# Kernel optimization log

Measured on AMD Instinct MI355X. Metric: run time of the kernel, lower is better.

The kernel has to match this reference:

```python
import jax, jax.numpy as jnp
from jax import lax
import numpy as np

MSS = 1448.0
MAX_RTT = 0.01
B, S = 2048, 4096


def setup_inputs() -> dict:
    key = jax.random.key(0)
    k1, k2, k3, k4 = jax.random.split(key, 4)
    # packet lengths in [0, 1500) bytes so bursts aggregate past MSS=1448
    x = jax.random.uniform(k1, (B, S), jnp.float32) * 1500.0
    mask = jax.random.uniform(k2, (B, S)) < 0.1
    scale = 0.00094557476340694
    d_exp = 1e-6 + scale * jax.random.exponential(k3, (B, S), jnp.float32)
    delays = jnp.where(mask, jnp.float32(0.21), d_exp)
    # per-burst RTT samples, indexed by the burst-start packet position
    rtts = jax.random.uniform(k4, (B, S), jnp.float32) * MAX_RTT
    return {"x": x, "delays": delays, "rtts": rtts}


def _simulate_row(x, delays, rtts):
    # x, delays, rtts: [S]
    S_ = x.shape[0]

    def step(carry, inp):
        active, new_burst, r = carry
        xj, dj, rj = inp
        # outer-while check only at burst start: stop forever if x[j] <= 0
        active = jnp.where(new_burst, active & (xj > 0), active)
        r = jnp.where(new_burst, rj, r)
        r_next = r - dj  # inner while: RTT -= delays[j]
        burst_end = active & (r_next <= 0)
        start_flag = new_burst & active
        return (active, burst_end, r_next), (active, start_flag)

    init = (jnp.bool_(True), jnp.bool_(True), jnp.float32(0.0))
    _, (consumed, start_flag) = lax.scan(step, init, (x, delays, rtts))

    # per-burst buffered byte count: segment-sum of consumed packet lengths
    burst_id = jnp.clip(jnp.cumsum(start_flag.astype(jnp.int32)) - 1, 0, S_ - 1)
    buf = jax.ops.segment_sum(jnp.where(consumed, x, 0.0), burst_id, num_segments=S_)

    # `while buf > MSS` emits ceil(buf/MSS)-1 full segments, then remainder
    n_full = jnp.maximum(jnp.ceil(buf / MSS).astype(jnp.int32) - 1, 0)
    rem = buf - n_full.astype(x.dtype) * MSS
    has_rem = rem > 0
    count = n_full + has_rem.astype(jnp.int32)
    starts = jnp.cumsum(count) - count  # exclusive cumsum: output offset per burst
    ends = starts + n_full

    # difference-array trick: positions in [starts, ends) get MSS (OOB drops == truncation)
    diff = (jnp.zeros(S_, jnp.int32)
            .at[starts].add(1, mode='drop')
            .at[ends].add(-1, mode='drop'))
    cover = jnp.cumsum(diff) > 0
    out = jnp.where(cover, jnp.float32(MSS), jnp.float32(0.0))

    # remainder goes right after the MSS run of its burst
    rem_pos = jnp.where(has_rem, ends, S_)  # S_ -> dropped
    out = out.at[rem_pos].set(rem, mode='drop')
    return out


def reference(x, delays, rtts):
    out = jax.vmap(_simulate_row)(x, delays, rtts)  # [B, S]
    return out[..., None]  # unsqueeze(-1) -> [B, S, 1]
```

## Files before the change

### kernel.cpp

```cpp
#include <hip/hip_runtime.h>
#include <math.h>


#define S_LEN 4096
#define BLOCK 512
#define PER   8
#define MSSF  1448.0f

#define OFF_A    0
#define OFF_JB   8208
#define OFF_NXT  16416
#define OFF_MENT 24616
#define OFF_WS   25640
#define SMEM_SZ  25672

__device__ __forceinline__ int s2i(int p) { return p ^ (((p >> 6) & 15) << 1); }

__global__ __launch_bounds__(BLOCK, 8) void traffic_kernel(
    const float* __restrict__ gx,
    const float* __restrict__ gd,
    const float* __restrict__ gr,
    float* __restrict__ gout)
{
    __shared__ __align__(16) unsigned char smem[SMEM_SZ];
    float*          s_dly  = (float*)(smem + OFF_A);
    unsigned short* s_jA   = (unsigned short*)(smem + OFF_A);
    unsigned short* s_jB   = (unsigned short*)(smem + OFF_JB);
    int*            s_diff = (int*)(smem + OFF_A);
    float*          s_out  = (float*)(smem + OFF_A);
    unsigned short* s_nxt  = (unsigned short*)(smem + OFF_NXT);
    unsigned short* s_ment = (unsigned short*)(smem + OFF_MENT);
    int*            s_ws   = (int*)(smem + OFF_WS);

    const int tid = threadIdx.x;
    const size_t rowoff = (size_t)blockIdx.x * S_LEN;
    const float* px = gx + rowoff;
    const float* pd = gd + rowoff;
    const float* pr = gr + rowoff;

    {
        const float4* pd4 = (const float4*)pd;
        float4* s4 = (float4*)s_dly;
        for (int q = tid; q < S_LEN / 4; q += BLOCK) s4[q] = pd4[q];
        if (tid < 8) s_dly[S_LEN + tid] = 1.0e30f;
    }
    float rt[PER];
    unsigned alive = 0;
#pragma unroll
    for (int i = 0; i < PER; ++i) rt[i] = pr[tid + (i << 9)];
#pragma unroll
    for (int i = 0; i < PER; ++i) alive |= (px[tid + (i << 9)] > 0.0f) ? (1u << i) : 0u;
    __syncthreads();

    unsigned surv = 0;
    float rsv[PER];
#pragma unroll
    for (int i = 0; i < PER; ++i) {
        const int p0 = tid + (i << 9);
        const float* dw = s_dly + p0;
        float d0 = dw[0], d1 = dw[1], d2 = dw[2], d3 = dw[3];
        float d4 = dw[4], d5 = dw[5], d6 = dw[6], d7 = dw[7];
        float r1 = rt[i] - d0;
        float r2 = r1 - d1;
        float r3 = r2 - d2;
        float r4 = r3 - d3;
        float r5 = r4 - d4;
        float r6 = r5 - d5;
        float r7 = r6 - d6;
        float r8 = r7 - d7;
        int c = (r1 > 0.0f) + (r2 > 0.0f) + (r3 > 0.0f) + (r4 > 0.0f) +
                (r5 > 0.0f) + (r6 > 0.0f) + (r7 > 0.0f) + (r8 > 0.0f);
        rsv[i] = r8;
        bool al = (alive >> i) & 1u;
        if (al && c == 8) {
            surv |= 1u << i;
        } else {
            int nx = al ? (p0 + c + 1) : S_LEN;
            if (nx > S_LEN) nx = S_LEN;
            s_nxt[s2i(p0)] = (unsigned short)nx;
        }
    }

    while (surv) {
        int i = __ffs(surv) - 1;
        surv &= surv - 1;
        float rr = rsv[0];
#pragma unroll
        for (int ii = 1; ii < PER; ++ii) rr = (i == ii) ? rsv[ii] : rr;
        int p0 = tid + (i << 9);
        int j = p0 + 8;
        int nx;
        while (true) {
            float e0 = s_dly[j],     e1 = s_dly[j + 1];
            float e2 = s_dly[j + 2], e3 = s_dly[j + 3];
            float e4 = s_dly[j + 4], e5 = s_dly[j + 5];
            float e6 = s_dly[j + 6], e7 = s_dly[j + 7];
            float q1 = rr - e0;
            float q2 = q1 - e1;
            float q3 = q2 - e2;
            float q4 = q3 - e3;
            float q5 = q4 - e4;
            float q6 = q5 - e5;
            float q7 = q6 - e6;
            float q8 = q7 - e7;
            int c2 = (q1 > 0.0f) + (q2 > 0.0f) + (q3 > 0.0f) + (q4 > 0.0f) +
                     (q5 > 0.0f) + (q6 > 0.0f) + (q7 > 0.0f) + (q8 > 0.0f);
            if (c2 < 8) { nx = j + c2 + 1; break; }
            j += 8;
            rr = q8;
        }
        if (nx > S_LEN) nx = S_LEN;
        s_nxt[s2i(p0)] = (unsigned short)nx;
    }
    __syncthreads();

    const int sb = tid << 3;
    {
        int nv[PER], ee[PER];
#pragma unroll
        for (int i = 0; i < PER; ++i) nv[i] = (int)s_nxt[s2i(sb + i)];
#pragma unroll
        for (int i = PER - 1; i >= 0; --i) {
            int v = nv[i];
            int e = v;
#pragma unroll
            for (int j2 = i + 1; j2 < PER; ++j2)
                if (v == sb + j2) e = ee[j2];
            ee[i] = e;
        }
        uint4 pk;
        pk.x = (unsigned)ee[0] | ((unsigned)ee[1] << 16);
        pk.y = (unsigned)ee[2] | ((unsigned)ee[3] << 16);
        pk.z = (unsigned)ee[4] | ((unsigned)ee[5] << 16);
        pk.w = (unsigned)ee[6] | ((unsigned)ee[7] << 16);
        *(uint4*)&s_jA[sb] = pk;
    }
    if (tid == 0) { s_jA[4096] = (unsigned short)4096; s_jB[4096] = (unsigned short)4096; }
    s_ment[tid] = (tid == 0) ? (unsigned short)1 : (unsigned short)0;
    __syncthreads();

    {
        unsigned short* ja = s_jA;
        unsigned short* jb = s_jB;
        int own[PER];
#pragma unroll
        for (int i = 0; i < PER; ++i) own[i] = (int)ja[tid + (i << 9)];
        for (int k = 0; k < 9; ++k) {
            int ent = (int)s_ment[tid];
            int q = -1;
            if (ent) {
                int e = (int)ja[ent - 1];
                if (e < S_LEN) q = e;
            }
            if (k < 8) {
                int nv[PER];
#pragma unroll
                for (int i = 0; i < PER; ++i) nv[i] = (int)ja[own[i]];
                if (q >= 0) s_ment[q >> 3] = (unsigned short)(q + 1);
#pragma unroll
                for (int i = 0; i < PER; ++i) jb[tid + (i << 9)] = (unsigned short)nv[i];
#pragma unroll
                for (int i = 0; i < PER; ++i) own[i] = nv[i];
            } else {
                if (q >= 0) s_ment[q >> 3] = (unsigned short)(q + 1);
            }
            __syncthreads();
            unsigned short* t = ja; ja = jb; jb = t;
        }
    }

    unsigned lm = 0;
    {
        int ent = (int)s_ment[tid];
        if (ent) {
            int p = ent - 1;
            while (p < sb + PER) {
                lm |= 1u << (p - sb);
                p = (int)s_nxt[s2i(p)];
            }
        }
    }

    float bsum[PER];
    unsigned use = 0;
    int tsum = 0;
#pragma unroll
    for (int i = 0; i < PER; ++i) {
        float buf = 0.0f;
        int c = 0;
        if ((lm >> i) & 1u) {
            int p = sb + i;
            float xp = px[p];
            if (xp > 0.0f) {
                use |= 1u << i;
                int e = (int)s_nxt[s2i(p)];
                float sum = xp;
                for (int j = p + 1; j < e; ++j) sum += px[j];
                buf = sum;
                int nf = (int)ceilf(buf / MSSF) - 1; if (nf < 0) nf = 0;
                float rem = buf - (float)nf * MSSF;
                c = nf + (rem > 0.0f ? 1 : 0);
            }
        }
        bsum[i] = buf;
        tsum += c;
    }

    int texcl;
    {
        int lane = tid & 63, wv = tid >> 6;
        int v = tsum;
        for (int off = 1; off < 64; off <<= 1) {
            int u = __shfl_up(v, off, 64);
            if (lane >= off) v += u;
        }
        if (lane == 63) s_ws[wv] = v;
        __syncthreads();
        int woff = 0;
        for (int w = 0; w < wv; ++w) woff += s_ws[w];
        texcl = woff + v - tsum;
    }

    {
        int4* d4 = (int4*)s_diff;
        int4 z; z.x = z.y = z.z = z.w = 0;
        d4[tid] = z;
        d4[tid + 512] = z;
    }
    __syncthreads();

    {
        int o = texcl;
#pragma unroll
        for (int i = 0; i < PER; ++i) {
            if ((use >> i) & 1u) {
                float buf = bsum[i];
                int nf = (int)ceilf(buf / MSSF) - 1; if (nf < 0) nf = 0;
                float rem = buf - (float)nf * MSSF;
                if (nf > 0) {
                    if (o < S_LEN) atomicAdd(&s_diff[o], 1);
                    int e2 = o + nf;
                    if (e2 < S_LEN) atomicAdd(&s_diff[e2], -1);
                }
                o += nf + (rem > 0.0f ? 1 : 0);
            }
        }
    }
    __syncthreads();

    {
        int4 a = *(int4*)&s_diff[sb];
        int4 b = *(int4*)&s_diff[sb + 4];
        int v0 = a.x,      v1 = v0 + a.y, v2 = v1 + a.z, v3 = v2 + a.w;
        int v4 = v3 + b.x, v5 = v4 + b.y, v6 = v5 + b.z, v7 = v6 + b.w;
        int T = v7;
        int lane = tid & 63, wv = tid >> 6;
        int sc = T;
        for (int off = 1; off < 64; off <<= 1) {
            int u = __shfl_up(sc, off, 64);
            if (lane >= off) sc += u;
        }
        if (lane == 63) s_ws[wv] = sc;
        __syncthreads();
        int basev = 0;
        for (int w = 0; w < wv; ++w) basev += s_ws[w];
        basev += sc - T;
        float4 fa, fb;
        fa.x = (basev + v0 > 0) ? MSSF : 0.0f;
        fa.y = (basev + v1 > 0) ? MSSF : 0.0f;
        fa.z = (basev + v2 > 0) ? MSSF : 0.0f;
        fa.w = (basev + v3 > 0) ? MSSF : 0.0f;
        fb.x = (basev + v4 > 0) ? MSSF : 0.0f;
        fb.y = (basev + v5 > 0) ? MSSF : 0.0f;
        fb.z = (basev + v6 > 0) ? MSSF : 0.0f;
        fb.w = (basev + v7 > 0) ? MSSF : 0.0f;
        *(float4*)&s_out[sb]     = fa;
        *(float4*)&s_out[sb + 4] = fb;
    }
    __syncthreads();

    {
        int o = texcl;
#pragma unroll
        for (int i = 0; i < PER; ++i) {
            if ((use >> i) & 1u) {
                float buf = bsum[i];
                int nf = (int)ceilf(buf / MSSF) - 1; if (nf < 0) nf = 0;
                float rem = buf - (float)nf * MSSF;
                int rp = o + nf;
                if (rem > 0.0f && rp < S_LEN) s_out[rp] = rem;
                o += nf + (rem > 0.0f ? 1 : 0);
            }
        }
    }
    __syncthreads();

    {
        float4* po4 = (float4*)(gout + rowoff);
        const float4* so4 = (const float4*)s_out;
        po4[tid]       = so4[tid];
        po4[tid + 512] = so4[tid + 512];
    }
}

extern "C" void kernel_launch(void* const* d_in, const int* in_sizes, int n_in,
                              void* d_out, int out_size, void* d_ws, size_t ws_size,
                              hipStream_t stream) {
    const float* x      = (const float*)d_in[0];
    const float* delays = (const float*)d_in[1];
    const float* rtts   = (const float*)d_in[2];
    float* out = (float*)d_out;
    int rows = in_sizes[0] / S_LEN;
    traffic_kernel<<<rows, BLOCK, 0, stream>>>(x, delays, rtts, out);
}
```

Before: 174.1 us.

## Keep per-thread packet lengths in registers, drop swizzle, pack next-pointers into nibbles

Each thread loads its 8 contiguous packet lengths once as float4 into registers. The alive test moves to after the next-pointer computation, and intra-thread burst sums use those registers instead of re-reading global memory. The XOR swizzle on s_nxt is removed so the 8 pointers load as one uint4. Local burst-start marking now walks a packed 4-bit relative-pointer word instead of chasing shared memory. The diff-array zeroing is moved before the scan so one barrier is dropped, which relies on the scan's internal sync for ordering and may bring back bank conflicts on the strided s_nxt writes.

Result: no change. 172.7 us (-0.8%).

```diff
diff --git a/kernel.cpp b/kernel.cpp
--- a/kernel.cpp
+++ b/kernel.cpp
@@ -10,11 +10,9 @@
 #define OFF_A    0
 #define OFF_JB   8208
 #define OFF_NXT  16416
-#define OFF_MENT 24616
-#define OFF_WS   25640
-#define SMEM_SZ  25672
-
-__device__ __forceinline__ int s2i(int p) { return p ^ (((p >> 6) & 15) << 1); }
+#define OFF_MENT 24624
+#define OFF_WS   25648
+#define SMEM_SZ  25680
 
 __global__ __launch_bounds__(BLOCK, 8) void traffic_kernel(
     const float* __restrict__ gx,
@@ -33,11 +31,19 @@
     int*            s_ws   = (int*)(smem + OFF_WS);
 
     const int tid = threadIdx.x;
+    const int sb  = tid << 3;
     const size_t rowoff = (size_t)blockIdx.x * S_LEN;
     const float* px = gx + rowoff;
     const float* pd = gd + rowoff;
     const float* pr = gr + rowoff;
 
+    float xreg[PER];
+    {
+        float4 xa = *(const float4*)(px + sb);
+        float4 xb = *(const float4*)(px + sb + 4);
+        xreg[0]=xa.x; xreg[1]=xa.y; xreg[2]=xa.z; xreg[3]=xa.w;
+        xreg[4]=xb.x; xreg[5]=xb.y; xreg[6]=xb.z; xreg[7]=xb.w;
+    }
     {
         const float4* pd4 = (const float4*)pd;
         float4* s4 = (float4*)s_dly;
@@ -45,11 +51,8 @@
         if (tid < 8) s_dly[S_LEN + tid] = 1.0e30f;
     }
     float rt[PER];
-    unsigned alive = 0;
 #pragma unroll
     for (int i = 0; i < PER; ++i) rt[i] = pr[tid + (i << 9)];
-#pragma unroll
-    for (int i = 0; i < PER; ++i) alive |= (px[tid + (i << 9)] > 0.0f) ? (1u << i) : 0u;
     __syncthreads();
 
     unsigned surv = 0;
@@ -71,13 +74,12 @@
         int c = (r1 > 0.0f) + (r2 > 0.0f) + (r3 > 0.0f) + (r4 > 0.0f) +
                 (r5 > 0.0f) + (r6 > 0.0f) + (r7 > 0.0f) + (r8 > 0.0f);
         rsv[i] = r8;
-        bool al = (alive >> i) & 1u;
-        if (al && c == 8) {
+        if (c == 8) {
             surv |= 1u << i;
         } else {
-            int nx = al ? (p0 + c + 1) : S_LEN;
+            int nx = p0 + c + 1;
             if (nx > S_LEN) nx = S_LEN;
-            s_nxt[s2i(p0)] = (unsigned short)nx;
+            s_nxt[p0] = (unsigned short)nx;
         }
     }
 
@@ -110,18 +112,25 @@
             rr = q8;
         }
         if (nx > S_LEN) nx = S_LEN;
-        s_nxt[s2i(p0)] = (unsigned short)nx;
-    }
-    __syncthreads();
-
-    const int sb = tid << 3;
-    {
-        int nv[PER], ee[PER];
-#pragma unroll
-        for (int i = 0; i < PER; ++i) nv[i] = (int)s_nxt[s2i(sb + i)];
+        s_nxt[p0] = (unsigned short)nx;
+    }
+    __syncthreads();
+
+    int nx8[PER];
+    unsigned long long rel = 0x8ull << 32;
+    {
+        uint4 ld = *(const uint4*)&s_nxt[sb];
+        nx8[0] = ld.x & 0xFFFF; nx8[1] = ld.x >> 16;
+        nx8[2] = ld.y & 0xFFFF; nx8[3] = ld.y >> 16;
+        nx8[4] = ld.z & 0xFFFF; nx8[5] = ld.z >> 16;
+        nx8[6] = ld.w & 0xFFFF; nx8[7] = ld.w >> 16;
+#pragma unroll
+        for (int i = 0; i < PER; ++i)
+            if (!(xreg[i] > 0.0f)) nx8[i] = S_LEN;
+        int ee[PER];
 #pragma unroll
         for (int i = PER - 1; i >= 0; --i) {
-            int v = nv[i];
+            int v = nx8[i];
             int e = v;
 #pragma unroll
             for (int j2 = i + 1; j2 < PER; ++j2)
@@ -134,6 +143,11 @@
         pk.z = (unsigned)ee[4] | ((unsigned)ee[5] << 16);
         pk.w = (unsigned)ee[6] | ((unsigned)ee[7] << 16);
         *(uint4*)&s_jA[sb] = pk;
+#pragma unroll
+        for (int i = 0; i < PER; ++i) {
+            int r = nx8[i] - sb; if (r > 8) r = 8;
+            rel |= (unsigned long long)r << (i << 2);
+        }
     }
     if (tid == 0) { s_jA[4096] = (unsigned short)4096; s_jB[4096] = (unsigned short)4096; }
     s_ment[tid] = (tid == 0) ? (unsigned short)1 : (unsigned short)0;
@@ -173,10 +187,11 @@
     {
         int ent = (int)s_ment[tid];
         if (ent) {
-            int p = ent - 1;
-            while (p < sb + PER) {
-                lm |= 1u << (p - sb);
-                p = (int)s_nxt[s2i(p)];
+            int p = ent - 1 - sb;
+#pragma unroll
+            for (int s = 0; s < PER; ++s) {
+                lm |= (p < 8) ? (1u << p) : 0u;
+                p = (int)((rel >> (p << 2)) & 15ull);
             }
         }
     }
@@ -189,13 +204,16 @@
         float buf = 0.0f;
         int c = 0;
         if ((lm >> i) & 1u) {
-            int p = sb + i;
-            float xp = px[p];
+            float xp = xreg[i];
             if (xp > 0.0f) {
                 use |= 1u << i;
-                int e = (int)s_nxt[s2i(p)];
+                int e = nx8[i];
+                int upper = e - sb;
                 float sum = xp;
-                for (int j = p + 1; j < e; ++j) sum += px[j];
+#pragma unroll
+                for (int jj = i + 1; jj < PER; ++jj)
+                    sum += (jj < upper) ? xreg[jj] : 0.0f;
+                for (int j = sb + PER; j < e; ++j) sum += px[j];
                 buf = sum;
                 int nf = (int)ceilf(buf / MSSF) - 1; if (nf < 0) nf = 0;
                 float rem = buf - (float)nf * MSSF;
@@ -206,6 +224,12 @@
         tsum += c;
     }
 
+    {
+        int4* d4 = (int4*)s_diff;
+        int4 z; z.x = z.y = z.z = z.w = 0;
+        d4[tid] = z;
+        d4[tid + 512] = z;
+    }
     int texcl;
     {
         int lane = tid & 63, wv = tid >> 6;
@@ -220,14 +244,6 @@
         for (int w = 0; w < wv; ++w) woff += s_ws[w];
         texcl = woff + v - tsum;
     }
-
-    {
-        int4* d4 = (int4*)s_diff;
-        int4 z; z.x = z.y = z.z = z.w = 0;
-        d4[tid] = z;
-        d4[tid + 512] = z;
-    }
-    __syncthreads();
 
     {
         int o = texcl;
```
